# Performance work log

Hardware: AMD Instinct MI355X
Metric: run time of the kernel (lower is better)

The kernel has to match this reference:

```python
import jax, jax.numpy as jnp
import numpy as np

N_NODES = 100000
N_EDGES = 1600000
EMB_DIM = 128
N_LAYERS = 3


def setup_inputs() -> dict:
    key = jax.random.key(0)
    k_emb, k_ws, k_wn, k_src, k_dst = jax.random.split(key, 5)
    scale = 1.0 / np.sqrt(EMB_DIM).astype(np.float32)
    emb_table = jax.random.normal(k_emb, (N_NODES, EMB_DIM), jnp.float32) * 0.02
    W_self = jax.random.normal(k_ws, (N_LAYERS, EMB_DIM, EMB_DIM), jnp.float32) * scale
    W_neigh = jax.random.normal(k_wn, (N_LAYERS, EMB_DIM, EMB_DIM), jnp.float32) * scale
    b = jnp.zeros((N_LAYERS, EMB_DIM), jnp.float32)
    src = jax.random.randint(k_src, (N_EDGES,), 0, N_NODES, jnp.int32)
    dst = jax.random.randint(k_dst, (N_EDGES,), 0, N_NODES, jnp.int32)
    return {"emb_table": emb_table, "W_self": W_self, "W_neigh": W_neigh,
            "b": b, "src": src, "dst": dst}


def reference(emb_table, W_self, W_neigh, b, src, dst):
    n = emb_table.shape[0]
    n_layers = W_self.shape[0]
    # in-degree per destination node, clamped to >=1 (DGL mean aggregator)
    deg = jax.ops.segment_sum(jnp.ones(src.shape[0], emb_table.dtype), dst, num_segments=n)
    inv_deg = (1.0 / jnp.maximum(deg, 1.0))[:, None]  # [N,1]
    x = emb_table
    for i in range(n_layers):
        # gather source features, mean-aggregate onto destinations
        neigh = jax.ops.segment_sum(x[src], dst, num_segments=n) * inv_deg  # [N,D]
        x = x @ W_self[i] + neigh @ W_neigh[i] + b[i]
        if i < n_layers - 1:
            x = jax.nn.relu(x)  # relu is idempotent: conv activation + outer relu
    return x
```

## Files before the change

### kernel.cpp

```cpp
#include <hip/hip_runtime.h>

#define EMB 128
#define CAP 64

typedef short bf16x8 __attribute__((ext_vector_type(8)));
typedef float f32x4 __attribute__((ext_vector_type(4)));
typedef int   i32x4 __attribute__((ext_vector_type(4)));

__device__ __forceinline__ float bf2f(unsigned int bits16) {
    return __uint_as_float(bits16 << 16);
}
__device__ __forceinline__ unsigned short f2bf(float f) {
    unsigned int u = __float_as_uint(f);
    u += 0x7FFF + ((u >> 16) & 1);
    return (unsigned short)(u >> 16);
}

__device__ __forceinline__ void gload_lds16(const void* g, void* l) {
    __builtin_amdgcn_global_load_lds((const __attribute__((address_space(1))) void*)g,
                                     (__attribute__((address_space(3))) void*)l,
                                     16, 0, 0);
}

__device__ __forceinline__ void place_edge(int ss, int dd, int lo, int hi,
                                           int* __restrict__ cnt, int* __restrict__ slot) {
    if (dd >= lo && dd < hi) {
        int pos = atomicAdd(&cnt[dd], 1);
        if (pos < CAP) slot[(size_t)dd * CAP + pos] = ss;
    }
}

__global__ void __launch_bounds__(256) scatter_pad_kernel(
        const int* __restrict__ src, const int* __restrict__ dst,
        int* __restrict__ cnt, int* __restrict__ slot, int e, int nr8, int n) {
    int r     = blockIdx.x & 7;
    int chunk = blockIdx.x >> 3;
    int lo = r * nr8;
    int hi = min(lo + nr8, n);
    int base = chunk * 1024 + (int)threadIdx.x * 4;
    if (base >= e) return;
    if (base + 4 <= e) {
        i32x4 s4 = __builtin_nontemporal_load((const i32x4*)(src + base));
        i32x4 d4 = __builtin_nontemporal_load((const i32x4*)(dst + base));
        place_edge(s4[0], d4[0], lo, hi, cnt, slot);
        place_edge(s4[1], d4[1], lo, hi, cnt, slot);
        place_edge(s4[2], d4[2], lo, hi, cnt, slot);
        place_edge(s4[3], d4[3], lo, hi, cnt, slot);
    } else {
        for (int i = base; i < e; ++i) place_edge(src[i], dst[i], lo, hi, cnt, slot);
    }
}

__global__ void cast_emb_kernel(const float* __restrict__ e,
                                unsigned short* __restrict__ xh, int total4) {
    int i = blockIdx.x * blockDim.x + threadIdx.x;
    if (i >= total4) return;
    float4 v = ((const float4*)e)[i];
    ushort4 o;
    o.x = f2bf(v.x); o.y = f2bf(v.y); o.z = f2bf(v.z); o.w = f2bf(v.w);
    ((ushort4*)xh)[i] = o;
}

__global__ void prep_w_kernel(const float* __restrict__ Ws, const float* __restrict__ Wn,
                              unsigned short* __restrict__ Wt, int total) {
    int i = blockIdx.x * blockDim.x + threadIdx.x;
    if (i >= total) return;
    int l   = i >> 15;
    int rem = i & 32767;
    int n   = rem >> 8;
    int kp  = rem & 255;
    int plane = kp >> 7;
    int kk    = kp & 127;
    const float* W = plane ? Wn : Ws;
    Wt[i] = f2bf(W[(size_t)l * EMB * EMB + kk * EMB + n]);
}

__global__ void __launch_bounds__(256) aggregate_bf_kernel(
        const unsigned short* __restrict__ xh, const int* __restrict__ cnt,
        const int* __restrict__ slot, unsigned short* __restrict__ nh, int n) {
    int node = blockIdx.x * 4 + (threadIdx.x >> 6);
    if (node >= n) return;
    int lane = threadIdx.x & 63;
    int half = lane >> 5;
    int col  = (lane & 31) * 4;
    int craw = cnt[node];
    int m = min(craw, CAP);
    int myslot = (lane < m) ? slot[(size_t)node * CAP + lane] : 0;
    float a0 = 0.f, a1 = 0.f, a2 = 0.f, a3 = 0.f;
    int j = 0;
    for (; j + 8 <= m; j += 8) {
        int r0 = __shfl(myslot, j + 0 + half);
        int r1 = __shfl(myslot, j + 2 + half);
        int r2 = __shfl(myslot, j + 4 + half);
        int r3 = __shfl(myslot, j + 6 + half);
        uint2 v0 = *(const uint2*)(xh + (size_t)r0 * EMB + col);
        uint2 v1 = *(const uint2*)(xh + (size_t)r1 * EMB + col);
        uint2 v2 = *(const uint2*)(xh + (size_t)r2 * EMB + col);
        uint2 v3 = *(const uint2*)(xh + (size_t)r3 * EMB + col);
        a0 += (bf2f(v0.x & 0xFFFFu) + bf2f(v1.x & 0xFFFFu)) + (bf2f(v2.x & 0xFFFFu) + bf2f(v3.x & 0xFFFFu));
        a1 += (bf2f(v0.x >> 16)     + bf2f(v1.x >> 16))     + (bf2f(v2.x >> 16)     + bf2f(v3.x >> 16));
        a2 += (bf2f(v0.y & 0xFFFFu) + bf2f(v1.y & 0xFFFFu)) + (bf2f(v2.y & 0xFFFFu) + bf2f(v3.y & 0xFFFFu));
        a3 += (bf2f(v0.y >> 16)     + bf2f(v1.y >> 16))     + (bf2f(v2.y >> 16)     + bf2f(v3.y >> 16));
    }
    for (; j + 2 <= m; j += 2) {
        int r0 = __shfl(myslot, j + half);
        uint2 v0 = *(const uint2*)(xh + (size_t)r0 * EMB + col);
        a0 += bf2f(v0.x & 0xFFFFu); a1 += bf2f(v0.x >> 16);
        a2 += bf2f(v0.y & 0xFFFFu); a3 += bf2f(v0.y >> 16);
    }
    int rl = __shfl(myslot, (m > 0) ? (m - 1) : 0);
    if ((m & 1) && half == 0) {
        uint2 v0 = *(const uint2*)(xh + (size_t)rl * EMB + col);
        a0 += bf2f(v0.x & 0xFFFFu); a1 += bf2f(v0.x >> 16);
        a2 += bf2f(v0.y & 0xFFFFu); a3 += bf2f(v0.y >> 16);
    }
    a0 += __shfl_xor(a0, 32); a1 += __shfl_xor(a1, 32);
    a2 += __shfl_xor(a2, 32); a3 += __shfl_xor(a3, 32);
    if (half == 0) {
        float sc = 1.0f / fmaxf((float)craw, 1.0f);
        uint2 o;
        o.x = (unsigned int)f2bf(a0 * sc) | ((unsigned int)f2bf(a1 * sc) << 16);
        o.y = (unsigned int)f2bf(a2 * sc) | ((unsigned int)f2bf(a3 * sc) << 16);
        *(uint2*)(nh + (size_t)node * EMB + col) = o;
    }
}

__global__ void __launch_bounds__(256) gemm_mfma_kernel(
        const unsigned short* __restrict__ xh, const unsigned short* __restrict__ nh,
        const unsigned short* __restrict__ Wt,
        const float* __restrict__ bias, float* __restrict__ outf,
        unsigned short* __restrict__ outh, int n, int do_relu) {
    __shared__ __align__(16) unsigned short a_s[128][64];
    __shared__ __align__(16) unsigned short b_s[128][64];

    int tid  = threadIdx.x;
    int w    = tid >> 6;
    int lane = tid & 63;
    int quad = lane >> 4;
    int l16  = lane & 15;
    int r7   = l16 & 7;
    int bm0  = blockIdx.x * 128;

    f32x4 acc[2][8];
    #pragma unroll
    for (int rt = 0; rt < 2; ++rt)
        #pragma unroll
        for (int ct = 0; ct < 8; ++ct)
            acc[rt][ct] = (f32x4){0.f, 0.f, 0.f, 0.f};

    for (int kc2 = 0; kc2 < 4; ++kc2) {
        const unsigned short* Ap = (kc2 < 2) ? xh : nh;
        int kk0 = (kc2 & 1) * 64;
        #pragma unroll
        for (int h = 0; h < 4; ++h) {
            int c   = tid + h * 256;
            int row = c >> 3;
            int s   = c & 7;
            int g   = s ^ (row & 7);
            int grr = bm0 + row; if (grr >= n) grr = n - 1;
            gload_lds16(Ap + (size_t)grr * EMB + kk0 + g * 8, &a_s[row][s * 8]);
            gload_lds16(Wt + (size_t)row * 256 + kc2 * 64 + g * 8, &b_s[row][s * 8]);
        }
        __syncthreads();
        #pragma unroll
        for (int ks = 0; ks < 2; ++ks) {
            int ca = ((ks * 4 + quad) ^ r7) * 8;
            bf16x8 af0 = *(const bf16x8*)&a_s[w * 32 + l16][ca];
            bf16x8 af1 = *(const bf16x8*)&a_s[w * 32 + 16 + l16][ca];
            #pragma unroll
            for (int ct = 0; ct < 8; ++ct) {
                bf16x8 bf = *(const bf16x8*)&b_s[ct * 16 + l16][ca];
                acc[0][ct] = __builtin_amdgcn_mfma_f32_16x16x32_bf16(af0, bf, acc[0][ct], 0, 0, 0);
                acc[1][ct] = __builtin_amdgcn_mfma_f32_16x16x32_bf16(af1, bf, acc[1][ct], 0, 0, 0);
            }
        }
        __syncthreads();
    }

    float bv[8];
    #pragma unroll
    for (int ct = 0; ct < 8; ++ct) bv[ct] = bias[ct * 16 + l16];
    #pragma unroll
    for (int rt = 0; rt < 2; ++rt) {
        #pragma unroll
        for (int r = 0; r < 4; ++r) {
            int grow = bm0 + w * 32 + rt * 16 + quad * 4 + r;
            if (grow >= n) continue;
            #pragma unroll
            for (int ct = 0; ct < 8; ++ct) {
                float v = acc[rt][ct][r] + bv[ct];
                if (do_relu) v = fmaxf(v, 0.f);
                int col = ct * 16 + l16;
                if (outf) outf[(size_t)grow * EMB + col] = v;
                else      outh[(size_t)grow * EMB + col] = f2bf(v);
            }
        }
    }
}

__global__ void hist_kernel(const int* __restrict__ dst, int* __restrict__ deg, int e) {
    int i = blockIdx.x * blockDim.x + threadIdx.x;
    int stride = gridDim.x * blockDim.x;
    for (; i < e; i += stride) atomicAdd(&deg[dst[i]], 1);
}

__global__ void __launch_bounds__(1024) scan_kernel(
        const int* __restrict__ deg, int* __restrict__ row_ptr,
        int* __restrict__ cursor, float* __restrict__ inv_deg, int n) {
    __shared__ int wave_tot[16];
    __shared__ int chunk_base_s;
    if (threadIdx.x == 0) chunk_base_s = 0;
    __syncthreads();
    int lane = threadIdx.x & 63;
    int wid  = threadIdx.x >> 6;
    for (int base = 0; base < n; base += 1024) {
        int i = base + (int)threadIdx.x;
        int v = (i < n) ? deg[i] : 0;
        int s = v;
        #pragma unroll
        for (int d = 1; d < 64; d <<= 1) {
            int t = __shfl_up(s, d, 64);
            if (lane >= d) s += t;
        }
        if (lane == 63) wave_tot[wid] = s;
        __syncthreads();
        int wsum = 0;
        for (int w2 = 0; w2 < wid; ++w2) wsum += wave_tot[w2];
        int excl = chunk_base_s + wsum + s - v;
        if (i < n) {
            row_ptr[i] = excl;
            cursor[i]  = excl;
            inv_deg[i] = 1.0f / fmaxf((float)v, 1.0f);
        }
        __syncthreads();
        if (threadIdx.x == 1023) chunk_base_s = excl + v;
        __syncthreads();
    }
    if (threadIdx.x == 0) row_ptr[n] = chunk_base_s;
}

__global__ void scatter_kernel(const int* __restrict__ src, const int* __restrict__ dst,
                               int* __restrict__ cursor, int* __restrict__ csr_src, int e) {
    int i = blockIdx.x * blockDim.x + threadIdx.x;
    if (i >= e) return;
    int d = dst[i];
    int pos = atomicAdd(&cursor[d], 1);
    csr_src[pos] = src[i];
}

__global__ void __launch_bounds__(256) aggregate_csr_kernel(
        const float* __restrict__ x, const int* __restrict__ row_ptr,
        const int* __restrict__ csr_src, const float* __restrict__ inv_deg,
        float* __restrict__ neigh, int n) {
    int node = blockIdx.x * 4 + (threadIdx.x >> 6);
    if (node >= n) return;
    int lane = threadIdx.x & 63;
    int beg = row_ptr[node];
    int end = row_ptr[node + 1];
    float ax = 0.f, ay = 0.f;
    for (int j = beg; j < end; ++j) {
        int s0 = csr_src[j];
        float2 v0 = *(const float2*)(x + (size_t)s0 * EMB + lane * 2);
        ax += v0.x;
        ay += v0.y;
    }
    float sc = inv_deg[node];
    *(float2*)(neigh + (size_t)node * EMB + lane * 2) = make_float2(ax * sc, ay * sc);
}

__global__ void __launch_bounds__(256) gemm_f32_kernel(
        const float* x, const float* __restrict__ neigh,
        const float* __restrict__ Ws, const float* __restrict__ Wn,
        const float* __restrict__ bias, float* out, int n, int do_relu) {
    __shared__ float s_ws[16][EMB];
    __shared__ float s_wn[16][EMB];
    __shared__ float s_x[16][68];
    __shared__ float s_n[16][68];
    int tid = threadIdx.x;
    int tc = tid & 31;
    int tr = tid >> 5;
    int bm0 = blockIdx.x * 64;
    float4 acc[8];
    #pragma unroll
    for (int r = 0; r < 8; ++r) acc[r] = make_float4(0.f, 0.f, 0.f, 0.f);
    for (int kc = 0; kc < 8; ++kc) {
        int k0 = kc * 16;
        const float4* wsv = (const float4*)(Ws + (size_t)k0 * EMB);
        const float4* wnv = (const float4*)(Wn + (size_t)k0 * EMB);
        ((float4*)s_ws)[tid] = wsv[tid];       ((float4*)s_ws)[tid + 256] = wsv[tid + 256];
        ((float4*)s_wn)[tid] = wnv[tid];       ((float4*)s_wn)[tid + 256] = wnv[tid + 256];
        int row = tid >> 2, kq = (tid & 3) * 4;
        int gr = bm0 + row;
        float4 vx = {0,0,0,0}, vn = {0,0,0,0};
        if (gr < n) {
            vx = *(const float4*)(x + (size_t)gr * EMB + k0 + kq);
            vn = *(const float4*)(neigh + (size_t)gr * EMB + k0 + kq);
        }
        s_x[kq+0][row] = vx.x; s_x[kq+1][row] = vx.y; s_x[kq+2][row] = vx.z; s_x[kq+3][row] = vx.w;
        s_n[kq+0][row] = vn.x; s_n[kq+1][row] = vn.y; s_n[kq+2][row] = vn.z; s_n[kq+3][row] = vn.w;
        __syncthreads();
        #pragma unroll
        for (int k = 0; k < 16; ++k) {
            float4 wa = *(const float4*)&s_ws[k][tc * 4];
            float4 wb = *(const float4*)&s_wn[k][tc * 4];
            float4 xv0 = *(const float4*)&s_x[k][tr * 8];
            float4 xv1 = *(const float4*)&s_x[k][tr * 8 + 4];
            float4 nv0 = *(const float4*)&s_n[k][tr * 8];
            float4 nv1 = *(const float4*)&s_n[k][tr * 8 + 4];
            #define ROWFMA(accv, xs, ns) \
                accv.x = fmaf(xs, wa.x, fmaf(ns, wb.x, accv.x)); \
                accv.y = fmaf(xs, wa.y, fmaf(ns, wb.y, accv.y)); \
                accv.z = fmaf(xs, wa.z, fmaf(ns, wb.z, accv.z)); \
                accv.w = fmaf(xs, wa.w, fmaf(ns, wb.w, accv.w));
            ROWFMA(acc[0], xv0.x, nv0.x) ROWFMA(acc[1], xv0.y, nv0.y)
            ROWFMA(acc[2], xv0.z, nv0.z) ROWFMA(acc[3], xv0.w, nv0.w)
            ROWFMA(acc[4], xv1.x, nv1.x) ROWFMA(acc[5], xv1.y, nv1.y)
            ROWFMA(acc[6], xv1.z, nv1.z) ROWFMA(acc[7], xv1.w, nv1.w)
            #undef ROWFMA
        }
        __syncthreads();
    }
    float4 bv = *(const float4*)(bias + tc * 4);
    #pragma unroll
    for (int r = 0; r < 8; ++r) {
        int gr = bm0 + tr * 8 + r;
        if (gr >= n) continue;
        float4 o = make_float4(acc[r].x + bv.x, acc[r].y + bv.y, acc[r].z + bv.z, acc[r].w + bv.w);
        if (do_relu) {
            o.x = fmaxf(o.x, 0.f); o.y = fmaxf(o.y, 0.f);
            o.z = fmaxf(o.z, 0.f); o.w = fmaxf(o.w, 0.f);
        }
        *(float4*)(out + (size_t)gr * EMB + tc * 4) = o;
    }
}

extern "C" void kernel_launch(void* const* d_in, const int* in_sizes, int n_in,
                              void* d_out, int out_size, void* d_ws, size_t ws_size,
                              hipStream_t stream) {
    const float* emb     = (const float*)d_in[0];
    const float* W_self  = (const float*)d_in[1];
    const float* W_neigh = (const float*)d_in[2];
    const float* bias    = (const float*)d_in[3];
    const int*   src     = (const int*)d_in[4];
    const int*   dst     = (const int*)d_in[5];
    const int N = in_sizes[0] / EMB;
    const int E = in_sizes[4];
    const int L = in_sizes[1] / (EMB * EMB);

    float* xout = (float*)d_out;

    auto align256 = [](size_t b) { return (b + 255) & ~(size_t)255; };
    size_t need_bf = align256((size_t)N * EMB * 2)
                   + align256((size_t)N * EMB * 2)
                   + align256((size_t)N * sizeof(int))
                   + align256((size_t)N * CAP * sizeof(int))
                   + align256((size_t)L * 32768 * 2);

    char* w = (char*)d_ws;
    auto alloc = [&](size_t bytes) {
        char* p = w;
        w += (bytes + 255) & ~(size_t)255;
        return p;
    };

    if (ws_size >= need_bf) {
        unsigned short* xh  = (unsigned short*)alloc((size_t)N * EMB * 2);
        unsigned short* nh  = (unsigned short*)alloc((size_t)N * EMB * 2);
        int*            cnt = (int*)alloc((size_t)N * sizeof(int));
        int*            slot= (int*)alloc((size_t)N * CAP * sizeof(int));
        unsigned short* Wt  = (unsigned short*)alloc((size_t)L * 32768 * 2);

        hipMemsetAsync(cnt, 0, (size_t)N * sizeof(int), stream);
        int nr8 = (N + 7) / 8;
        int chunks = (E + 1023) / 1024;
        scatter_pad_kernel<<<chunks * 8, 256, 0, stream>>>(src, dst, cnt, slot, E, nr8, N);
        cast_emb_kernel<<<(N * EMB / 4 + 255) / 256, 256, 0, stream>>>(emb, xh, N * EMB / 4);
        prep_w_kernel<<<(L * 32768 + 255) / 256, 256, 0, stream>>>(W_self, W_neigh, Wt, L * 32768);

        int gg = (N + 127) / 128;
        for (int l = 0; l < L; ++l) {
            aggregate_bf_kernel<<<(N + 3) / 4, 256, 0, stream>>>(xh, cnt, slot, nh, N);
            int last = (l == L - 1);
            gemm_mfma_kernel<<<gg, 256, 0, stream>>>(
                xh, nh, Wt + (size_t)l * 32768, bias + (size_t)l * EMB,
                last ? xout : nullptr, last ? nullptr : xh, N, last ? 0 : 1);
        }
    } else {
        float* neigh   = (float*)alloc((size_t)N * EMB * sizeof(float));
        int*   deg     = (int*)  alloc((size_t)N * sizeof(int));
        int*   row_ptr = (int*)  alloc((size_t)(N + 1) * sizeof(int));
        int*   cursor  = (int*)  alloc((size_t)N * sizeof(int));
        float* inv_deg = (float*)alloc((size_t)N * sizeof(float));
        int*   csr     = (int*)  alloc((size_t)E * sizeof(int));

        hipMemsetAsync(deg, 0, (size_t)N * sizeof(int), stream);
        hist_kernel<<<2048, 256, 0, stream>>>(dst, deg, E);
        scan_kernel<<<1, 1024, 0, stream>>>(deg, row_ptr, cursor, inv_deg, N);
        scatter_kernel<<<(E + 255) / 256, 256, 0, stream>>>(src, dst, cursor, csr, E);

        for (int l = 0; l < L; ++l) {
            const float* xin = (l == 0) ? emb : xout;
            aggregate_csr_kernel<<<(N + 3) / 4, 256, 0, stream>>>(xin, row_ptr, csr, inv_deg, neigh, N);
            gemm_f32_kernel<<<(N + 63) / 64, 256, 0, stream>>>(
                xin, neigh,
                W_self + (size_t)l * EMB * EMB, W_neigh + (size_t)l * EMB * EMB,
                bias + (size_t)l * EMB, xout, N, (l < L - 1) ? 1 : 0);
        }
    }
}
```

Measured before the change: 430.8 us.

## Fuse neighbor aggregation into the per-layer MFMA GEMM via an LDS tile

The separate aggregate kernel is removed. Each 128-row GEMM block now gathers and mean-reduces the neighbor features of its own rows into a swizzled 32KB LDS tile and feeds that tile to the MFMA loop for the W_neigh half. This avoids writing and re-reading the bf16 neighbor matrix in global memory, and saves one launch per layer. Because other blocks still read the previous layer's features, the layers now ping-pong between two bf16 buffers. The risk is that the latency-bound gather now runs inside only a few hundred blocks, each using 64KB of LDS, so there is far less occupancy to hide gather latency. The scatter kernel also drops its nontemporal loads in favor of plain int4 loads.

```diff
diff --git a/kernel.cpp b/kernel.cpp
--- a/kernel.cpp
+++ b/kernel.cpp
@@ -5,7 +5,6 @@
 
 typedef short bf16x8 __attribute__((ext_vector_type(8)));
 typedef float f32x4 __attribute__((ext_vector_type(4)));
-typedef int   i32x4 __attribute__((ext_vector_type(4)));
 
 __device__ __forceinline__ float bf2f(unsigned int bits16) {
     return __uint_as_float(bits16 << 16);
@@ -40,12 +39,12 @@
     int base = chunk * 1024 + (int)threadIdx.x * 4;
     if (base >= e) return;
     if (base + 4 <= e) {
-        i32x4 s4 = __builtin_nontemporal_load((const i32x4*)(src + base));
-        i32x4 d4 = __builtin_nontemporal_load((const i32x4*)(dst + base));
-        place_edge(s4[0], d4[0], lo, hi, cnt, slot);
-        place_edge(s4[1], d4[1], lo, hi, cnt, slot);
-        place_edge(s4[2], d4[2], lo, hi, cnt, slot);
-        place_edge(s4[3], d4[3], lo, hi, cnt, slot);
+        int4 s4 = *(const int4*)(src + base);
+        int4 d4 = *(const int4*)(dst + base);
+        place_edge(s4.x, d4.x, lo, hi, cnt, slot);
+        place_edge(s4.y, d4.y, lo, hi, cnt, slot);
+        place_edge(s4.z, d4.z, lo, hi, cnt, slot);
+        place_edge(s4.w, d4.w, lo, hi, cnt, slot);
     } else {
         for (int i = base; i < e; ++i) place_edge(src[i], dst[i], lo, hi, cnt, slot);
     }
@@ -75,61 +74,13 @@
     Wt[i] = f2bf(W[(size_t)l * EMB * EMB + kk * EMB + n]);
 }
 
-__global__ void __launch_bounds__(256) aggregate_bf_kernel(
-        const unsigned short* __restrict__ xh, const int* __restrict__ cnt,
-        const int* __restrict__ slot, unsigned short* __restrict__ nh, int n) {
-    int node = blockIdx.x * 4 + (threadIdx.x >> 6);
-    if (node >= n) return;
-    int lane = threadIdx.x & 63;
-    int half = lane >> 5;
-    int col  = (lane & 31) * 4;
-    int craw = cnt[node];
-    int m = min(craw, CAP);
-    int myslot = (lane < m) ? slot[(size_t)node * CAP + lane] : 0;
-    float a0 = 0.f, a1 = 0.f, a2 = 0.f, a3 = 0.f;
-    int j = 0;
-    for (; j + 8 <= m; j += 8) {
-        int r0 = __shfl(myslot, j + 0 + half);
-        int r1 = __shfl(myslot, j + 2 + half);
-        int r2 = __shfl(myslot, j + 4 + half);
-        int r3 = __shfl(myslot, j + 6 + half);
-        uint2 v0 = *(const uint2*)(xh + (size_t)r0 * EMB + col);
-        uint2 v1 = *(const uint2*)(xh + (size_t)r1 * EMB + col);
-        uint2 v2 = *(const uint2*)(xh + (size_t)r2 * EMB + col);
-        uint2 v3 = *(const uint2*)(xh + (size_t)r3 * EMB + col);
-        a0 += (bf2f(v0.x & 0xFFFFu) + bf2f(v1.x & 0xFFFFu)) + (bf2f(v2.x & 0xFFFFu) + bf2f(v3.x & 0xFFFFu));
-        a1 += (bf2f(v0.x >> 16)     + bf2f(v1.x >> 16))     + (bf2f(v2.x >> 16)     + bf2f(v3.x >> 16));
-        a2 += (bf2f(v0.y & 0xFFFFu) + bf2f(v1.y & 0xFFFFu)) + (bf2f(v2.y & 0xFFFFu) + bf2f(v3.y & 0xFFFFu));
-        a3 += (bf2f(v0.y >> 16)     + bf2f(v1.y >> 16))     + (bf2f(v2.y >> 16)     + bf2f(v3.y >> 16));
-    }
-    for (; j + 2 <= m; j += 2) {
-        int r0 = __shfl(myslot, j + half);
-        uint2 v0 = *(const uint2*)(xh + (size_t)r0 * EMB + col);
-        a0 += bf2f(v0.x & 0xFFFFu); a1 += bf2f(v0.x >> 16);
-        a2 += bf2f(v0.y & 0xFFFFu); a3 += bf2f(v0.y >> 16);
-    }
-    int rl = __shfl(myslot, (m > 0) ? (m - 1) : 0);
-    if ((m & 1) && half == 0) {
-        uint2 v0 = *(const uint2*)(xh + (size_t)rl * EMB + col);
-        a0 += bf2f(v0.x & 0xFFFFu); a1 += bf2f(v0.x >> 16);
-        a2 += bf2f(v0.y & 0xFFFFu); a3 += bf2f(v0.y >> 16);
-    }
-    a0 += __shfl_xor(a0, 32); a1 += __shfl_xor(a1, 32);
-    a2 += __shfl_xor(a2, 32); a3 += __shfl_xor(a3, 32);
-    if (half == 0) {
-        float sc = 1.0f / fmaxf((float)craw, 1.0f);
-        uint2 o;
-        o.x = (unsigned int)f2bf(a0 * sc) | ((unsigned int)f2bf(a1 * sc) << 16);
-        o.y = (unsigned int)f2bf(a2 * sc) | ((unsigned int)f2bf(a3 * sc) << 16);
-        *(uint2*)(nh + (size_t)node * EMB + col) = o;
-    }
-}
-
-__global__ void __launch_bounds__(256) gemm_mfma_kernel(
-        const unsigned short* __restrict__ xh, const unsigned short* __restrict__ nh,
+__global__ void __launch_bounds__(256) layer_fused_kernel(
+        const unsigned short* __restrict__ xin,
+        const int* __restrict__ cnt, const int* __restrict__ slot,
         const unsigned short* __restrict__ Wt,
         const float* __restrict__ bias, float* __restrict__ outf,
         unsigned short* __restrict__ outh, int n, int do_relu) {
+    __shared__ __align__(16) unsigned short n_s[128][128];
     __shared__ __align__(16) unsigned short a_s[128][64];
     __shared__ __align__(16) unsigned short b_s[128][64];
 
@@ -141,6 +92,57 @@
     int r7   = l16 & 7;
     int bm0  = blockIdx.x * 128;
 
+    int half = lane >> 5;
+    int c4   = (lane & 31) * 4;
+    int ch   = (lane & 31) >> 1;
+    int sub  = c4 & 7;
+    for (int i = 0; i < 32; ++i) {
+        int nb   = i * 4 + w;
+        int node = bm0 + nb;
+        if (node >= n) continue;
+        int craw = cnt[node];
+        int m = min(craw, CAP);
+        int myslot = (lane < m) ? slot[(size_t)node * CAP + lane] : 0;
+        float a0 = 0.f, a1 = 0.f, a2 = 0.f, a3 = 0.f;
+        int j = 0;
+        for (; j + 8 <= m; j += 8) {
+            int r0 = __shfl(myslot, j + 0 + half);
+            int r1 = __shfl(myslot, j + 2 + half);
+            int r2 = __shfl(myslot, j + 4 + half);
+            int r3 = __shfl(myslot, j + 6 + half);
+            uint2 v0 = *(const uint2*)(xin + (size_t)r0 * EMB + c4);
+            uint2 v1 = *(const uint2*)(xin + (size_t)r1 * EMB + c4);
+            uint2 v2 = *(const uint2*)(xin + (size_t)r2 * EMB + c4);
+            uint2 v3 = *(const uint2*)(xin + (size_t)r3 * EMB + c4);
+            a0 += (bf2f(v0.x & 0xFFFFu) + bf2f(v1.x & 0xFFFFu)) + (bf2f(v2.x & 0xFFFFu) + bf2f(v3.x & 0xFFFFu));
+            a1 += (bf2f(v0.x >> 16)     + bf2f(v1.x >> 16))     + (bf2f(v2.x >> 16)     + bf2f(v3.x >> 16));
+            a2 += (bf2f(v0.y & 0xFFFFu) + bf2f(v1.y & 0xFFFFu)) + (bf2f(v2.y & 0xFFFFu) + bf2f(v3.y & 0xFFFFu));
+            a3 += (bf2f(v0.y >> 16)     + bf2f(v1.y >> 16))     + (bf2f(v2.y >> 16)     + bf2f(v3.y >> 16));
+        }
+        for (; j + 2 <= m; j += 2) {
+            int r0 = __shfl(myslot, j + half);
+            uint2 v0 = *(const uint2*)(xin + (size_t)r0 * EMB + c4);
+            a0 += bf2f(v0.x & 0xFFFFu); a1 += bf2f(v0.x >> 16);
+            a2 += bf2f(v0.y & 0xFFFFu); a3 += bf2f(v0.y >> 16);
+        }
+        int rl = __shfl(myslot, (m > 0) ? (m - 1) : 0);
+        if ((m & 1) && half == 0) {
+            uint2 v0 = *(const uint2*)(xin + (size_t)rl * EMB + c4);
+            a0 += bf2f(v0.x & 0xFFFFu); a1 += bf2f(v0.x >> 16);
+            a2 += bf2f(v0.y & 0xFFFFu); a3 += bf2f(v0.y >> 16);
+        }
+        a0 += __shfl_xor(a0, 32); a1 += __shfl_xor(a1, 32);
+        a2 += __shfl_xor(a2, 32); a3 += __shfl_xor(a3, 32);
+        if (half == 0) {
+            float sc = 1.0f / fmaxf((float)craw, 1.0f);
+            uint2 o;
+            o.x = (unsigned int)f2bf(a0 * sc) | ((unsigned int)f2bf(a1 * sc) << 16);
+            o.y = (unsigned int)f2bf(a2 * sc) | ((unsigned int)f2bf(a3 * sc) << 16);
+            int col = (ch ^ (nb & 7)) * 8 + sub;
+            *(uint2*)&n_s[nb][col] = o;
+        }
+    }
+
     f32x4 acc[2][8];
     #pragma unroll
     for (int rt = 0; rt < 2; ++rt)
@@ -149,27 +151,46 @@
             acc[rt][ct] = (f32x4){0.f, 0.f, 0.f, 0.f};
 
     for (int kc2 = 0; kc2 < 4; ++kc2) {
-        const unsigned short* Ap = (kc2 < 2) ? xh : nh;
-        int kk0 = (kc2 & 1) * 64;
-        #pragma unroll
-        for (int h = 0; h < 4; ++h) {
-            int c   = tid + h * 256;
-            int row = c >> 3;
-            int s   = c & 7;
-            int g   = s ^ (row & 7);
-            int grr = bm0 + row; if (grr >= n) grr = n - 1;
-            gload_lds16(Ap + (size_t)grr * EMB + kk0 + g * 8, &a_s[row][s * 8]);
-            gload_lds16(Wt + (size_t)row * 256 + kc2 * 64 + g * 8, &b_s[row][s * 8]);
+        if (kc2 < 2) {
+            int kk0 = kc2 * 64;
+            #pragma unroll
+            for (int h = 0; h < 4; ++h) {
+                int c   = tid + h * 256;
+                int row = c >> 3;
+                int s   = c & 7;
+                int g   = s ^ (row & 7);
+                int grr = bm0 + row; if (grr >= n) grr = n - 1;
+                gload_lds16(xin + (size_t)grr * EMB + kk0 + g * 8, &a_s[row][s * 8]);
+                gload_lds16(Wt + (size_t)row * 256 + kc2 * 64 + g * 8, &b_s[row][s * 8]);
+            }
+        } else {
+            #pragma unroll
+            for (int h = 0; h < 4; ++h) {
+                int c   = tid + h * 256;
+                int row = c >> 3;
+                int s   = c & 7;
+                int g   = s ^ (row & 7);
+                gload_lds16(Wt + (size_t)row * 256 + kc2 * 64 + g * 8, &b_s[row][s * 8]);
+            }
         }
         __syncthreads();
         #pragma unroll
         for (int ks = 0; ks < 2; ++ks) {
-            int ca = ((ks * 4 + quad) ^ r7) * 8;
-            bf16x8 af0 = *(const bf16x8*)&a_s[w * 32 + l16][ca];
-            bf16x8 af1 = *(const bf16x8*)&a_s[w * 32 + 16 + l16][ca];
+            int cb = ((ks * 4 + quad) ^ r7) * 8;
+            bf16x8 af0, af1;
+            if (kc2 < 2) {
+                af0 = *(const bf16x8*)&a_s[w * 32 + l16][cb];
+                af1 = *(const bf16x8*)&a_s[w * 32 + 16 + l16][cb];
+            } else if (kc2 == 2) {
+                af0 = *(const bf16x8*)&n_s[w * 32 + l16][cb];
+                af1 = *(const bf16x8*)&n_s[w * 32 + 16 + l16][cb];
+            } else {
+                af0 = *(const bf16x8*)&n_s[w * 32 + l16][64 + cb];
+                af1 = *(const bf16x8*)&n_s[w * 32 + 16 + l16][64 + cb];
+            }
             #pragma unroll
             for (int ct = 0; ct < 8; ++ct) {
-                bf16x8 bf = *(const bf16x8*)&b_s[ct * 16 + l16][ca];
+                bf16x8 bf = *(const bf16x8*)&b_s[ct * 16 + l16][cb];
                 acc[0][ct] = __builtin_amdgcn_mfma_f32_16x16x32_bf16(af0, bf, acc[0][ct], 0, 0, 0);
                 acc[1][ct] = __builtin_amdgcn_mfma_f32_16x16x32_bf16(af1, bf, acc[1][ct], 0, 0, 0);
             }
@@ -364,8 +385,8 @@
     };
 
     if (ws_size >= need_bf) {
-        unsigned short* xh  = (unsigned short*)alloc((size_t)N * EMB * 2);
-        unsigned short* nh  = (unsigned short*)alloc((size_t)N * EMB * 2);
+        unsigned short* xh0 = (unsigned short*)alloc((size_t)N * EMB * 2);
+        unsigned short* xh1 = (unsigned short*)alloc((size_t)N * EMB * 2);
         int*            cnt = (int*)alloc((size_t)N * sizeof(int));
         int*            slot= (int*)alloc((size_t)N * CAP * sizeof(int));
         unsigned short* Wt  = (unsigned short*)alloc((size_t)L * 32768 * 2);
@@ -374,16 +395,18 @@
         int nr8 = (N + 7) / 8;
         int chunks = (E + 1023) / 1024;
         scatter_pad_kernel<<<chunks * 8, 256, 0, stream>>>(src, dst, cnt, slot, E, nr8, N);
-        cast_emb_kernel<<<(N * EMB / 4 + 255) / 256, 256, 0, stream>>>(emb, xh, N * EMB / 4);
+        cast_emb_kernel<<<(N * EMB / 4 + 255) / 256, 256, 0, stream>>>(emb, xh0, N * EMB / 4);
         prep_w_kernel<<<(L * 32768 + 255) / 256, 256, 0, stream>>>(W_self, W_neigh, Wt, L * 32768);
 
         int gg = (N + 127) / 128;
+        const unsigned short* cur = xh0;
+        unsigned short*       nxt = xh1;
         for (int l = 0; l < L; ++l) {
-            aggregate_bf_kernel<<<(N + 3) / 4, 256, 0, stream>>>(xh, cnt, slot, nh, N);
             int last = (l == L - 1);
-            gemm_mfma_kernel<<<gg, 256, 0, stream>>>(
-                xh, nh, Wt + (size_t)l * 32768, bias + (size_t)l * EMB,
-                last ? xout : nullptr, last ? nullptr : xh, N, last ? 0 : 1);
+            layer_fused_kernel<<<gg, 256, 0, stream>>>(
+                cur, cnt, slot, Wt + (size_t)l * 32768, bias + (size_t)l * EMB,
+                last ? xout : nullptr, last ? nullptr : nxt, N, last ? 0 : 1);
+            const unsigned short* t = cur; cur = nxt; nxt = (unsigned short*)t;
         }
     } else {
         float* neigh   = (float*)alloc((size_t)N * EMB * sizeof(float));
```

Measured after the change: 687.0 us. 59.5% more time.
